# Kernel optimization log

Hardware: AMD Instinct MI355X
Metric: run time of the kernel (lower is better)

Reference implementation:

```python
import jax, jax.numpy as jnp
from jax import lax
import numpy as np

GAMMA = 1e-4  # RBF bandwidth (init kwarg gamma)

def setup_inputs() -> dict:
    key = jax.random.key(0)
    ks = jax.random.split(key, 6)
    B, H, W = 2048, 64, 64
    P, D = 4096, 4096  # D = 4 * (H//2) * (W//2)
    NC = 10
    x = jax.random.normal(ks[0], (B, 1, H, W), dtype=jnp.float32)
    prototypes = jax.random.normal(ks[1], (P, D), dtype=jnp.float32) * 0.5
    conv_w = jax.random.normal(ks[2], (4, 1, 2, 2), dtype=jnp.float32) * 0.5
    conv_b = jax.random.normal(ks[3], (4,), dtype=jnp.float32) * 0.1
    head_w = jax.random.normal(ks[4], (NC, P), dtype=jnp.float32) * (1.0 / np.sqrt(P))
    head_b = jax.random.normal(ks[5], (NC,), dtype=jnp.float32) * 0.1
    return {"x": x, "prototypes": prototypes, "conv_w": conv_w,
            "conv_b": conv_b, "head_w": head_w, "head_b": head_b}

def reference(x, prototypes, conv_w, conv_b, head_w, head_b):
    # 2x2 stride-2 conv: [B,1,H,W] -> [B,4,H/2,W/2]
    feats = lax.conv_general_dilated(
        x, conv_w, window_strides=(2, 2), padding="VALID",
        dimension_numbers=("NCHW", "OIHW", "NCHW"))
    feats = feats + conv_b[None, :, None, None]
    B = feats.shape[0]
    feats = feats.reshape(B, -1)  # [B, D]
    # Pairwise squared distance via ||f||^2 + ||p||^2 - 2 f.p (no [B,P,D] blowup)
    f2 = jnp.sum(feats * feats, axis=1, keepdims=True)          # [B,1]
    p2 = jnp.sum(prototypes * prototypes, axis=1)[None, :]      # [1,P]
    d2 = jnp.maximum(f2 + p2 - 2.0 * feats @ prototypes.T, 0.0)  # [B,P]
    kernel_vals = jnp.exp(-GAMMA * d2)
    logits = kernel_vals @ head_w.T + head_b
    return jax.nn.log_softmax(logits, axis=-1)
```

## Files before the change

### kernel.cpp

```cpp
#include <hip/hip_runtime.h>
#include <hip/hip_bf16.h>
#include <stdint.h>

#define GAMMA 1e-4f

typedef int i32x4 __attribute__((ext_vector_type(4)));
typedef int i32x8 __attribute__((ext_vector_type(8)));
typedef float f32x4 __attribute__((ext_vector_type(4)));

__device__ __forceinline__ float bf2f(unsigned short u) {
  unsigned int x = ((unsigned int)u) << 16;
  float f; __builtin_memcpy(&f, &x, 4);
  return f;
}

__device__ __forceinline__ unsigned char f2e4m3(float x) {
  float a = fabsf(x);
  unsigned char s = x < 0.f ? 0x80 : 0;
  a = fminf(a, 448.f);
  if (a < 0.015625f) {
    int q = (int)rintf(a * 512.f);
    return s | (unsigned char)q;
  }
  unsigned int u; __builtin_memcpy(&u, &a, 4);
  u += 0x7FFFFu + ((u >> 20) & 1);
  u &= 0xFFF00000u;
  int e2 = (int)(u >> 23) - 127;
  unsigned int mant = (u >> 20) & 7;
  return s | (unsigned char)(((e2 + 7) << 3) | mant);
}

__device__ __forceinline__ unsigned int pack4(float a, float b, float c, float d) {
  return (unsigned)f2e4m3(a) | ((unsigned)f2e4m3(b) << 8) |
         ((unsigned)f2e4m3(c) << 16) | ((unsigned)f2e4m3(d) << 24);
}

__global__ __launch_bounds__(256) void prep_k(
    const float* __restrict__ x, const float* __restrict__ cw,
    const float* __restrict__ cb, unsigned char* __restrict__ fA8,
    float* __restrict__ f2, const float* __restrict__ pr,
    unsigned char* __restrict__ pB8, float* __restrict__ p2) {
  const int tid = threadIdx.x;
  __shared__ float red[4];
  if (blockIdx.x < 4096) {
    const int j = blockIdx.x;
    const float4* src = (const float4*)(pr + (size_t)j * 4096);
    float ssq = 0.f;
    unsigned int w4[4];
#pragma unroll
    for (int k = 0; k < 4; k++) {
      float4 v = src[tid * 4 + k];
      ssq += v.x * v.x + v.y * v.y + v.z * v.z + v.w * v.w;
      w4[k] = pack4(v.x, v.y, v.z, v.w);
    }
    *(uint4*)(pB8 + (size_t)j * 4096 + tid * 16) = make_uint4(w4[0], w4[1], w4[2], w4[3]);
    for (int off = 32; off > 0; off >>= 1) ssq += __shfl_down(ssq, off);
    if ((tid & 63) == 0) red[tid >> 6] = ssq;
    __syncthreads();
    if (tid == 0) p2[j] = red[0] + red[1] + red[2] + red[3];
  } else {
    const int b = blockIdx.x - 4096;
    __shared__ float swb[20];
    if (tid < 16) swb[tid] = cw[tid];
    else if (tid < 20) swb[tid] = cb[tid - 16];
    __syncthreads();
    float w[16], bias[4];
#pragma unroll
    for (int i = 0; i < 16; i++) w[i] = swb[i];
#pragma unroll
    for (int c = 0; c < 4; c++) bias[c] = swb[16 + c];
    const float* xb = x + (size_t)b * 4096;
    unsigned char* fb8 = fA8 + (size_t)b * 4096;
    const int p0 = tid * 4;
    const int h = p0 >> 5, w0 = p0 & 31;
    const float* r0 = xb + (2 * h) * 64 + 2 * w0;
    const float* r1 = r0 + 64;
    float4 a0 = *(const float4*)r0, a1 = *(const float4*)(r0 + 4);
    float4 c0 = *(const float4*)r1, c1 = *(const float4*)(r1 + 4);
    float ssq = 0.f;
#pragma unroll
    for (int c = 0; c < 4; c++) {
      float w00 = w[c * 4], w01 = w[c * 4 + 1], w10 = w[c * 4 + 2], w11 = w[c * 4 + 3];
      float v0 = bias[c] + a0.x * w00 + a0.y * w01 + c0.x * w10 + c0.y * w11;
      float v1 = bias[c] + a0.z * w00 + a0.w * w01 + c0.z * w10 + c0.w * w11;
      float v2 = bias[c] + a1.x * w00 + a1.y * w01 + c1.x * w10 + c1.y * w11;
      float v3 = bias[c] + a1.z * w00 + a1.w * w01 + c1.z * w10 + c1.w * w11;
      ssq += v0 * v0 + v1 * v1 + v2 * v2 + v3 * v3;
      *(unsigned int*)(fb8 + c * 1024 + p0) = pack4(v0, v1, v2, v3);
    }
    for (int off = 32; off > 0; off >>= 1) ssq += __shfl_down(ssq, off);
    if ((tid & 63) == 0) red[tid >> 6] = ssq;
    __syncthreads();
    if (tid == 0) f2[b] = red[0] + red[1] + red[2] + red[3];
  }
}

#define SWZA(o) ((o) ^ ((((o) >> 12) & 1) << 4))
#define SWZB(o) ((o) ^ ((((o) >> 13) & 1) << 4))
#define TILE_BYTES 49152

#define GLDS(gsrc, ldst)                                                    \
  __builtin_amdgcn_global_load_lds(                                         \
      (__attribute__((address_space(1))) void*)(void*)(gsrc),               \
      (__attribute__((address_space(3))) void*)(ldst), 16, 0, 0)

#define MFMA8(a, b, c)                                                      \
  __builtin_amdgcn_mfma_scale_f32_16x16x128_f8f6f4(                         \
      (a), (b), (c), 0, 0, 0, 0x7f7f7f7fu, 0, 0x7f7f7f7fu)

__device__ __forceinline__ i32x8 read32(const char* p0, const char* p1) {
  i32x4 lo = *(const i32x4*)p0;
  i32x4 hi = *(const i32x4*)p1;
  return __builtin_shufflevector(lo, hi, 0, 1, 2, 3, 4, 5, 6, 7);
}

#define SB __builtin_amdgcn_sched_barrier(0)
#define LGKM0 asm volatile("s_waitcnt lgkmcnt(0)" ::: "memory")

#define TBODY(CUR, STG, KB)                                                 \
  {                                                                         \
    i32x8 av0, av1, av2, av3, bv0, bv1, bv2, bv3;                           \
                                                \
    SB;                                                                     \
    av0 = read32((CUR) + arlo[0], (CUR) + arhi[0]);                         \
    av1 = read32((CUR) + arlo[1], (CUR) + arhi[1]);                         \
    bv0 = read32((CUR) + brlo[0], (CUR) + brhi[0]);                         \
    bv1 = read32((CUR) + brlo[1], (CUR) + brhi[1]);                         \
    SB;                                                                     \
    GLDS(agp[0] + (KB), (STG) + aoff[0]);                                   \
    GLDS(agp[1] + (KB), (STG) + aoff[1]);                                   \
    SB;                                                                     \
    __builtin_amdgcn_s_barrier();                                           \
    LGKM0; SB;                                                              \
    __builtin_amdgcn_s_setprio(1);                                          \
    acc[0][0] = MFMA8(av0, bv0, acc[0][0]);                                 \
    acc[0][1] = MFMA8(av0, bv1, acc[0][1]);                                 \
    acc[1][0] = MFMA8(av1, bv0, acc[1][0]);                                 \
    acc[1][1] = MFMA8(av1, bv1, acc[1][1]);                                 \
    __builtin_amdgcn_s_setprio(0);                                          \
    SB;                                                                     \
                                                \
    av2 = read32((CUR) + arlo[2], (CUR) + arhi[2]);                         \
    av3 = read32((CUR) + arlo[3], (CUR) + arhi[3]);                         \
    SB;                                                                     \
    GLDS(bgp[0] + (KB), (STG) + 16384 + boff[0]);                           \
    GLDS(bgp[1] + (KB), (STG) + 16384 + boff[1]);                           \
    SB;                                                                     \
    __builtin_amdgcn_s_barrier();                                           \
    LGKM0; SB;                                                              \
    __builtin_amdgcn_s_setprio(1);                                          \
    acc[2][0] = MFMA8(av2, bv0, acc[2][0]);                                 \
    acc[2][1] = MFMA8(av2, bv1, acc[2][1]);                                 \
    acc[3][0] = MFMA8(av3, bv0, acc[3][0]);                                 \
    acc[3][1] = MFMA8(av3, bv1, acc[3][1]);                                 \
    __builtin_amdgcn_s_setprio(0);                                          \
    SB;                                                                     \
                                                \
    bv2 = read32((CUR) + brlo[2], (CUR) + brhi[2]);                         \
    bv3 = read32((CUR) + brlo[3], (CUR) + brhi[3]);                         \
    SB;                                                                     \
    GLDS(bgp[2] + (KB), (STG) + 16384 + boff[2]);                           \
    GLDS(bgp[3] + (KB), (STG) + 16384 + boff[3]);                           \
    SB;                                                                     \
    __builtin_amdgcn_s_barrier();                                           \
    LGKM0; SB;                                                              \
    __builtin_amdgcn_s_setprio(1);                                          \
    acc[0][2] = MFMA8(av0, bv2, acc[0][2]);                                 \
    acc[0][3] = MFMA8(av0, bv3, acc[0][3]);                                 \
    acc[1][2] = MFMA8(av1, bv2, acc[1][2]);                                 \
    acc[1][3] = MFMA8(av1, bv3, acc[1][3]);                                 \
    __builtin_amdgcn_s_setprio(0);                                          \
    SB;                                                                     \
                                   \
    __builtin_amdgcn_s_barrier();                                           \
    __builtin_amdgcn_s_setprio(1);                                          \
    acc[2][2] = MFMA8(av2, bv2, acc[2][2]);                                 \
    acc[2][3] = MFMA8(av2, bv3, acc[2][3]);                                 \
    acc[3][2] = MFMA8(av3, bv2, acc[3][2]);                                 \
    acc[3][3] = MFMA8(av3, bv3, acc[3][3]);                                 \
    __builtin_amdgcn_s_setprio(0);                                          \
    SB;                                                                     \
    asm volatile("s_waitcnt vmcnt(6)" ::: "memory");                        \
    SB;                                                                     \
    __builtin_amdgcn_s_barrier();                                           \
  }

__global__ __launch_bounds__(512, 1) void gemm_kv_k(
    const unsigned char* __restrict__ A, const unsigned char* __restrict__ B,
    const float* __restrict__ f2, const float* __restrict__ p2,
    __hip_bfloat16* __restrict__ kv) {
  __shared__ __align__(16) char lds[3 * TILE_BYTES];
  const int tid = threadIdx.x;
  const int wave = tid >> 6, lane = tid & 63;
  const int q = lane >> 4, l16 = lane & 15;
  const int wr = wave >> 2, wc = wave & 3;

  const int wg = blockIdx.x;
  const int xcd = wg & 7, loc = wg >> 3;
  const int bm = (xcd & 1) * 8 + (loc & 7);
  const int bn = (xcd >> 1) * 4 + (loc >> 3);

  const unsigned char* agp[2];
  const unsigned char* bgp[4];
  int aoff[2], boff[4];
#pragma unroll
  for (int i = 0; i < 2; i++) {
    int phys = (tid + i * 512) * 16;
    aoff[i] = phys;
    int lg = SWZA(phys);
    int kq = lg >> 12, rw = (lg & 4095) >> 5, kl = lg & 31;
    agp[i] = A + (size_t)(bm * 128 + rw) * 4096 + kq * 32 + kl;
  }
#pragma unroll
  for (int i = 0; i < 4; i++) {
    int phys = (tid + i * 512) * 16;
    boff[i] = phys;
    int lg = SWZB(phys);
    int kq = lg >> 13, rw = (lg & 8191) >> 5, kl = lg & 31;
    bgp[i] = B + (size_t)(bn * 256 + rw) * 4096 + kq * 32 + kl;
  }

  int arlo[4], arhi[4], brlo[4], brhi[4];
#pragma unroll
  for (int m = 0; m < 4; m++) {
    int lg = q * 4096 + (wr * 64 + m * 16 + l16) * 32;
    arlo[m] = SWZA(lg);
    arhi[m] = SWZA(lg + 16);
  }
#pragma unroll
  for (int n = 0; n < 4; n++) {
    int lg = q * 8192 + (wc * 64 + n * 16 + l16) * 32;
    brlo[n] = 16384 + SWZB(lg);
    brhi[n] = 16384 + SWZB(lg + 16);
  }

  f32x4 acc[4][4] = {};

  char* b0 = lds;
  char* b1 = lds + TILE_BYTES;
  char* b2 = lds + 2 * TILE_BYTES;

#pragma unroll
  for (int i = 0; i < 2; i++) GLDS(agp[i], b0 + aoff[i]);
#pragma unroll
  for (int i = 0; i < 4; i++) GLDS(bgp[i], b0 + 16384 + boff[i]);
#pragma unroll
  for (int i = 0; i < 2; i++) GLDS(agp[i] + 128, b1 + aoff[i]);
#pragma unroll
  for (int i = 0; i < 4; i++) GLDS(bgp[i] + 128, b1 + 16384 + boff[i]);
  asm volatile("s_waitcnt vmcnt(6)" ::: "memory");
  __builtin_amdgcn_s_barrier();

#pragma unroll 1
  for (int t = 0; t < 32; ++t) {
    const int kb2 = ((t + 2) & 31) * 128;
    TBODY(b0, b2, kb2);
    char* nb0 = b1; char* nb1 = b2; char* nb2 = b0;
    b0 = nb0; b1 = nb1; b2 = nb2;
  }

  asm volatile("s_waitcnt vmcnt(0) lgkmcnt(0)" ::: "memory");

  float p2v[4];
#pragma unroll
  for (int n = 0; n < 4; n++) p2v[n] = p2[bn * 256 + wc * 64 + n * 16 + l16];
#pragma unroll
  for (int m = 0; m < 4; m++) {
#pragma unroll
    for (int j = 0; j < 4; j++) {
      int grow = bm * 128 + wr * 64 + m * 16 + q * 4 + j;
      float f2v = f2[grow];
      __hip_bfloat16* kvp = kv + (size_t)grow * 4096 + bn * 256 + wc * 64 + l16;
#pragma unroll
      for (int n = 0; n < 4; n++) {
        float d2 = fmaxf(f2v + p2v[n] - 2.0f * acc[m][n][j], 0.f);
        kvp[n * 16] = __float2bfloat16(__expf(-GAMMA * d2));
      }
    }
  }
}

__global__ __launch_bounds__(256, 4) void head_ls_k(
    const __hip_bfloat16* __restrict__ kv, const float* __restrict__ hw,
    const float* __restrict__ hb, float* __restrict__ out) {
  const int bb = blockIdx.x * 4;
  const int tid = threadIdx.x;
  float part[4][10];
#pragma unroll
  for (int r = 0; r < 4; r++)
#pragma unroll
    for (int c = 0; c < 10; c++) part[r][c] = 0.f;

#pragma unroll 1
  for (int k = 0; k < 4; k++) {
    const int idx = tid + k * 256;
    float a[4][4];
#pragma unroll
    for (int r = 0; r < 4; r++) {
      ushort4 v = ((const ushort4*)(kv + (size_t)(bb + r) * 4096))[idx];
      a[r][0] = bf2f(v.x); a[r][1] = bf2f(v.y); a[r][2] = bf2f(v.z); a[r][3] = bf2f(v.w);
    }
#pragma unroll
    for (int c = 0; c < 10; c++) {
      float4 w = *(const float4*)(hw + c * 4096 + idx * 4);
#pragma unroll
      for (int r = 0; r < 4; r++)
        part[r][c] += a[r][0] * w.x + a[r][1] * w.y + a[r][2] * w.z + a[r][3] * w.w;
    }
  }

#pragma unroll
  for (int r = 0; r < 4; r++)
#pragma unroll
    for (int c = 0; c < 10; c++)
      for (int off = 32; off > 0; off >>= 1) part[r][c] += __shfl_down(part[r][c], off);

  __shared__ float red[4][4][10];
  if ((tid & 63) == 0) {
#pragma unroll
    for (int r = 0; r < 4; r++)
#pragma unroll
      for (int c = 0; c < 10; c++) red[tid >> 6][r][c] = part[r][c];
  }
  __syncthreads();
  if (tid < 4) {
    const int r = tid;
    float l[10], m = -1e30f;
#pragma unroll
    for (int c = 0; c < 10; c++) {
      l[c] = red[0][r][c] + red[1][r][c] + red[2][r][c] + red[3][r][c] + hb[c];
      m = fmaxf(m, l[c]);
    }
    float s = 0.f;
#pragma unroll
    for (int c = 0; c < 10; c++) s += __expf(l[c] - m);
    float lse = logf(s);
#pragma unroll
    for (int c = 0; c < 10; c++) out[(size_t)(bb + r) * 10 + c] = l[c] - m - lse;
  }
}

extern "C" void kernel_launch(void* const* d_in, const int* in_sizes, int n_in,
                              void* d_out, int out_size, void* d_ws, size_t ws_size,
                              hipStream_t stream) {
  const float* x      = (const float*)d_in[0];
  const float* protos = (const float*)d_in[1];
  const float* conv_w = (const float*)d_in[2];
  const float* conv_b = (const float*)d_in[3];
  const float* head_w = (const float*)d_in[4];
  const float* head_b = (const float*)d_in[5];
  float* out = (float*)d_out;
  char* ws = (char*)d_ws;

  unsigned char* pB8  = (unsigned char*)ws;
  unsigned char* fA8  = (unsigned char*)(ws + (16u << 20));
  __hip_bfloat16* kvb = (__hip_bfloat16*)(ws + (24u << 20));
  float* f2 = (float*)(ws + (40u << 20));
  float* p2 = (float*)(ws + (40u << 20) + 8192);

  hipLaunchKernelGGL(prep_k, dim3(6144), dim3(256), 0, stream,
                     x, conv_w, conv_b, fA8, f2, protos, pB8, p2);
  hipLaunchKernelGGL(gemm_kv_k, dim3(256), dim3(512), 0, stream, fA8, pB8, f2, p2, kvb);
  hipLaunchKernelGGL(head_ls_k, dim3(512), dim3(256), 0, stream, kvb, head_w, head_b, out);
}
```

Baseline: 80.80 us.

## Load A fragments straight from global into registers, keep only B in LDS

The A operand of the fp8 GEMM is no longer staged through LDS. Each wave now reads its A fragments directly from global memory into double-buffered registers, one step ahead, while B keeps the triple-buffered global-to-LDS path. This shrinks the LDS tile, removes the A LDS reads and several barriers per iteration, and unrolls the loop by two to alternate the register sets. The cost is more VGPRs and more global traffic, since A is now read per wave instead of shared across waves. The vmcnt/lgkmcnt wait counts are hand-tuned and carry a risk of a correctness race.

```diff
diff --git a/kernel.cpp b/kernel.cpp
--- a/kernel.cpp
+++ b/kernel.cpp
@@ -95,9 +95,8 @@
   }
 }
 
-#define SWZA(o) ((o) ^ ((((o) >> 12) & 1) << 4))
 #define SWZB(o) ((o) ^ ((((o) >> 13) & 1) << 4))
-#define TILE_BYTES 49152
+#define TILE_BYTES 32768
 
 #define GLDS(gsrc, ldst)                                                    \
   __builtin_amdgcn_global_load_lds(                                         \
@@ -113,74 +112,61 @@
   i32x4 hi = *(const i32x4*)p1;
   return __builtin_shufflevector(lo, hi, 0, 1, 2, 3, 4, 5, 6, 7);
 }
+__device__ __forceinline__ i32x8 read_a(const unsigned char* p) {
+  i32x4 lo = *(const i32x4*)p;
+  i32x4 hi = *(const i32x4*)(p + 16);
+  return __builtin_shufflevector(lo, hi, 0, 1, 2, 3, 4, 5, 6, 7);
+}
 
 #define SB __builtin_amdgcn_sched_barrier(0)
-#define LGKM0 asm volatile("s_waitcnt lgkmcnt(0)" ::: "memory")
-
-#define TBODY(CUR, STG, KB)                                                 \
+
+#define TBODY(CUR, STG, AX0, AX1, AX2, AX3, KB)                             \
   {                                                                         \
-    i32x8 av0, av1, av2, av3, bv0, bv1, bv2, bv3;                           \
-                                                \
-    SB;                                                                     \
-    av0 = read32((CUR) + arlo[0], (CUR) + arhi[0]);                         \
-    av1 = read32((CUR) + arlo[1], (CUR) + arhi[1]);                         \
+    i32x8 bv0, bv1, bv2, bv3;                                               \
+    SB;                                                                     \
     bv0 = read32((CUR) + brlo[0], (CUR) + brhi[0]);                         \
     bv1 = read32((CUR) + brlo[1], (CUR) + brhi[1]);                         \
     SB;                                                                     \
-    GLDS(agp[0] + (KB), (STG) + aoff[0]);                                   \
-    GLDS(agp[1] + (KB), (STG) + aoff[1]);                                   \
-    SB;                                                                     \
-    __builtin_amdgcn_s_barrier();                                           \
-    LGKM0; SB;                                                              \
-    __builtin_amdgcn_s_setprio(1);                                          \
-    acc[0][0] = MFMA8(av0, bv0, acc[0][0]);                                 \
-    acc[0][1] = MFMA8(av0, bv1, acc[0][1]);                                 \
-    acc[1][0] = MFMA8(av1, bv0, acc[1][0]);                                 \
-    acc[1][1] = MFMA8(av1, bv1, acc[1][1]);                                 \
-    __builtin_amdgcn_s_setprio(0);                                          \
-    SB;                                                                     \
-                                                \
-    av2 = read32((CUR) + arlo[2], (CUR) + arhi[2]);                         \
-    av3 = read32((CUR) + arlo[3], (CUR) + arhi[3]);                         \
-    SB;                                                                     \
-    GLDS(bgp[0] + (KB), (STG) + 16384 + boff[0]);                           \
-    GLDS(bgp[1] + (KB), (STG) + 16384 + boff[1]);                           \
-    SB;                                                                     \
-    __builtin_amdgcn_s_barrier();                                           \
-    LGKM0; SB;                                                              \
-    __builtin_amdgcn_s_setprio(1);                                          \
-    acc[2][0] = MFMA8(av2, bv0, acc[2][0]);                                 \
-    acc[2][1] = MFMA8(av2, bv1, acc[2][1]);                                 \
-    acc[3][0] = MFMA8(av3, bv0, acc[3][0]);                                 \
-    acc[3][1] = MFMA8(av3, bv1, acc[3][1]);                                 \
-    __builtin_amdgcn_s_setprio(0);                                          \
-    SB;                                                                     \
-                                                \
+    GLDS(bgp[0] + (KB), (STG) + boff[0]);                                   \
+    GLDS(bgp[1] + (KB), (STG) + boff[1]);                                   \
+    GLDS(bgp[2] + (KB), (STG) + boff[2]);                                   \
+    GLDS(bgp[3] + (KB), (STG) + boff[3]);                                   \
+    SB;                                                                     \
     bv2 = read32((CUR) + brlo[2], (CUR) + brhi[2]);                         \
     bv3 = read32((CUR) + brlo[3], (CUR) + brhi[3]);                         \
     SB;                                                                     \
-    GLDS(bgp[2] + (KB), (STG) + 16384 + boff[2]);                           \
-    GLDS(bgp[3] + (KB), (STG) + 16384 + boff[3]);                           \
-    SB;                                                                     \
-    __builtin_amdgcn_s_barrier();                                           \
-    LGKM0; SB;                                                              \
+    asm volatile("s_waitcnt lgkmcnt(4)" ::: "memory");                      \
+    SB;                                                                     \
     __builtin_amdgcn_s_setprio(1);                                          \
-    acc[0][2] = MFMA8(av0, bv2, acc[0][2]);                                 \
-    acc[0][3] = MFMA8(av0, bv3, acc[0][3]);                                 \
-    acc[1][2] = MFMA8(av1, bv2, acc[1][2]);                                 \
-    acc[1][3] = MFMA8(av1, bv3, acc[1][3]);                                 \
+    acc[0][0] = MFMA8(AX0, bv0, acc[0][0]);                                 \
+    acc[0][1] = MFMA8(AX0, bv1, acc[0][1]);                                 \
+    acc[1][0] = MFMA8(AX1, bv0, acc[1][0]);                                 \
+    acc[1][1] = MFMA8(AX1, bv1, acc[1][1]);                                 \
+    acc[2][0] = MFMA8(AX2, bv0, acc[2][0]);                                 \
+    acc[2][1] = MFMA8(AX2, bv1, acc[2][1]);                                 \
+    acc[3][0] = MFMA8(AX3, bv0, acc[3][0]);                                 \
+    acc[3][1] = MFMA8(AX3, bv1, acc[3][1]);                                 \
     __builtin_amdgcn_s_setprio(0);                                          \
     SB;                                                                     \
-                                   \
-    __builtin_amdgcn_s_barrier();                                           \
+    asm volatile("s_waitcnt lgkmcnt(0)" ::: "memory");                      \
+    SB;                                                                     \
     __builtin_amdgcn_s_setprio(1);                                          \
-    acc[2][2] = MFMA8(av2, bv2, acc[2][2]);                                 \
-    acc[2][3] = MFMA8(av2, bv3, acc[2][3]);                                 \
-    acc[3][2] = MFMA8(av3, bv2, acc[3][2]);                                 \
-    acc[3][3] = MFMA8(av3, bv3, acc[3][3]);                                 \
+    acc[0][2] = MFMA8(AX0, bv2, acc[0][2]);                                 \
+    acc[0][3] = MFMA8(AX0, bv3, acc[0][3]);                                 \
+    acc[1][2] = MFMA8(AX1, bv2, acc[1][2]);                                 \
+    acc[1][3] = MFMA8(AX1, bv3, acc[1][3]);                                 \
+    acc[2][2] = MFMA8(AX2, bv2, acc[2][2]);                                 \
+    acc[2][3] = MFMA8(AX2, bv3, acc[2][3]);                                 \
+    acc[3][2] = MFMA8(AX3, bv2, acc[3][2]);                                 \
+    acc[3][3] = MFMA8(AX3, bv3, acc[3][3]);                                 \
     __builtin_amdgcn_s_setprio(0);                                          \
     SB;                                                                     \
-    asm volatile("s_waitcnt vmcnt(6)" ::: "memory");                        \
+    AX0 = read_a(ag[0] + (KB));    \
+    AX1 = read_a(ag[1] + (KB));                                             \
+    AX2 = read_a(ag[2] + (KB));                                             \
+    AX3 = read_a(ag[3] + (KB));                                             \
+    SB;                                                                     \
+    asm volatile("s_waitcnt vmcnt(12)" ::: "memory");                       \
     SB;                                                                     \
     __builtin_amdgcn_s_barrier();                                           \
   }
@@ -200,17 +186,8 @@
   const int bm = (xcd & 1) * 8 + (loc & 7);
   const int bn = (xcd >> 1) * 4 + (loc >> 3);
 
-  const unsigned char* agp[2];
   const unsigned char* bgp[4];
-  int aoff[2], boff[4];
-#pragma unroll
-  for (int i = 0; i < 2; i++) {
-    int phys = (tid + i * 512) * 16;
-    aoff[i] = phys;
-    int lg = SWZA(phys);
-    int kq = lg >> 12, rw = (lg & 4095) >> 5, kl = lg & 31;
-    agp[i] = A + (size_t)(bm * 128 + rw) * 4096 + kq * 32 + kl;
-  }
+  int boff[4];
 #pragma unroll
   for (int i = 0; i < 4; i++) {
     int phys = (tid + i * 512) * 16;
@@ -220,43 +197,46 @@
     bgp[i] = B + (size_t)(bn * 256 + rw) * 4096 + kq * 32 + kl;
   }
 
-  int arlo[4], arhi[4], brlo[4], brhi[4];
-#pragma unroll
-  for (int m = 0; m < 4; m++) {
-    int lg = q * 4096 + (wr * 64 + m * 16 + l16) * 32;
-    arlo[m] = SWZA(lg);
-    arhi[m] = SWZA(lg + 16);
-  }
+  int brlo[4], brhi[4];
 #pragma unroll
   for (int n = 0; n < 4; n++) {
     int lg = q * 8192 + (wc * 64 + n * 16 + l16) * 32;
-    brlo[n] = 16384 + SWZB(lg);
-    brhi[n] = 16384 + SWZB(lg + 16);
-  }
+    brlo[n] = SWZB(lg);
+    brhi[n] = SWZB(lg + 16);
+  }
+
+  const unsigned char* ag[4];
+#pragma unroll
+  for (int m = 0; m < 4; m++)
+    ag[m] = A + (size_t)(bm * 128 + wr * 64 + m * 16 + l16) * 4096 + q * 32;
 
   f32x4 acc[4][4] = {};
+  i32x8 Xa0, Xa1, Xa2, Xa3, Ya0, Ya1, Ya2, Ya3;
 
   char* b0 = lds;
   char* b1 = lds + TILE_BYTES;
   char* b2 = lds + 2 * TILE_BYTES;
 
 #pragma unroll
-  for (int i = 0; i < 2; i++) GLDS(agp[i], b0 + aoff[i]);
-#pragma unroll
-  for (int i = 0; i < 4; i++) GLDS(bgp[i], b0 + 16384 + boff[i]);
-#pragma unroll
-  for (int i = 0; i < 2; i++) GLDS(agp[i] + 128, b1 + aoff[i]);
-#pragma unroll
-  for (int i = 0; i < 4; i++) GLDS(bgp[i] + 128, b1 + 16384 + boff[i]);
-  asm volatile("s_waitcnt vmcnt(6)" ::: "memory");
+  for (int i = 0; i < 4; i++) GLDS(bgp[i], b0 + boff[i]);
+#pragma unroll
+  for (int i = 0; i < 4; i++) GLDS(bgp[i] + 128, b1 + boff[i]);
+  Xa0 = read_a(ag[0]); Xa1 = read_a(ag[1]); Xa2 = read_a(ag[2]); Xa3 = read_a(ag[3]);
+  Ya0 = read_a(ag[0] + 128); Ya1 = read_a(ag[1] + 128);
+  Ya2 = read_a(ag[2] + 128); Ya3 = read_a(ag[3] + 128);
+  SB;
+  asm volatile("s_waitcnt vmcnt(16)" ::: "memory");
+  SB;
   __builtin_amdgcn_s_barrier();
 
 #pragma unroll 1
-  for (int t = 0; t < 32; ++t) {
-    const int kb2 = ((t + 2) & 31) * 128;
-    TBODY(b0, b2, kb2);
-    char* nb0 = b1; char* nb1 = b2; char* nb2 = b0;
-    b0 = nb0; b1 = nb1; b2 = nb2;
+  for (int t = 0; t < 32; t += 2) {
+    const int kb0 = ((t + 2) & 31) * 128;
+    const int kb1 = ((t + 3) & 31) * 128;
+    TBODY(b0, b2, Xa0, Xa1, Xa2, Xa3, kb0);
+    TBODY(b1, b0, Ya0, Ya1, Ya2, Ya3, kb1);
+    char* n0 = b2; char* n1 = b0; char* n2 = b1;
+    b0 = n0; b1 = n1; b2 = n2;
   }
 
   asm volatile("s_waitcnt vmcnt(0) lgkmcnt(0)" ::: "memory");
```

Result: slower. 126.5 us (+56.6%).
